# Optimization experiments

Measured on AMD Instinct MI355X. Metric: run time of the kernel, lower is better.

The kernel has to match this reference:

```python
import jax, jax.numpy as jnp
import numpy as np
from jax import lax

B, C, H, W = 4, 256, 64, 64
C8 = C // 8  # 32


def setup_inputs() -> dict:
    key = jax.random.key(0)
    ks = jax.random.split(key, 8)
    x = jax.random.normal(ks[0], (B, C, H, W), jnp.float32)
    # 1x1 conv weights stored as [out_ch, in_ch]
    wb = jax.random.normal(ks[1], (C8, 2 * C), jnp.float32) * 0.02
    bb = jax.random.normal(ks[2], (C8,), jnp.float32) * 0.02
    wc = jax.random.normal(ks[3], (C8, 2 * C), jnp.float32) * 0.02
    bc = jax.random.normal(ks[4], (C8,), jnp.float32) * 0.02
    wd = jax.random.normal(ks[5], (C, 2 * C), jnp.float32) * 0.02
    bd = jax.random.normal(ks[6], (C,), jnp.float32) * 0.02
    alpha = jnp.float32(0.5)  # nn.Parameter(zeros(1)) at init; nonzero for a meaningful test
    return {"x": x, "wb": wb, "bb": bb, "wc": wc, "bc": bc, "wd": wd, "bd": bd, "alpha": alpha}


def reference(x, wb, bb, wc, bc, wd, bd, alpha):
    b, c, h, w = x.shape
    n = h * w
    pad = [(0, 0), (0, 0), (1, 1), (1, 1)]
    # F.avg_pool2d(k=3, s=1, p=1) with count_include_pad=True -> window-sum / 9
    x_avg = lax.reduce_window(x, 0.0, lax.add, (1, 1, 3, 3), (1, 1, 1, 1), pad) / 9.0
    x_max = lax.reduce_window(x, -jnp.inf, lax.max, (1, 1, 3, 3), (1, 1, 1, 1), pad)
    cat = jnp.concatenate([x_avg, x_max], axis=1)  # [B, 2C, H, W]
    catf = cat.reshape(b, 2 * c, n)                # [B, 2C, N]
    # 1x1 convs == per-pixel linear projections
    feat_b = jnp.einsum('oc,bcn->bon', wb, catf) + bb[None, :, None]  # [B, C8, N]
    feat_c = jnp.einsum('oc,bcn->bon', wc, catf) + bc[None, :, None]  # [B, C8, N]
    feat_d = jnp.einsum('oc,bcn->bon', wd, catf) + bd[None, :, None]  # [B, C,  N]
    # attention_s = softmax(feat_b^T @ feat_c) over last dim -> [B, N, N]
    attn = jax.nn.softmax(jnp.einsum('bon,bom->bnm', feat_b, feat_c), axis=-1)
    # feat_e = feat_d @ attn^T -> [B, C, N]
    feat_e = jnp.einsum('bcn,bmn->bcm', feat_d, attn).reshape(b, c, h, w)
    return alpha * feat_e + (1.0 - alpha) * x
```

## Files before the change

### kernel.cpp

```cpp
#include <hip/hip_runtime.h>
#include <hip/hip_bf16.h>

typedef __hip_bfloat16 bf16;
typedef __attribute__((ext_vector_type(8))) short s8v;
typedef __attribute__((ext_vector_type(4))) float f4v;

__device__ __forceinline__ ushort f2u(float f) {
    bf16 h = __float2bfloat16(f);
    return *(ushort*)&h;
}


__global__ __launch_bounds__(256) void wcvt_kernel(
    const float* __restrict__ wb, const float* __restrict__ wc,
    const float* __restrict__ wd, ushort* __restrict__ Wf) {
    int f = blockIdx.x * 4 + (threadIdx.x >> 6);
    int l = threadIdx.x & 63;
    int ot = f % 20, kc = f / 20;
    int o = ot * 16 + (l & 15);
    int k0 = kc * 32 + (l >> 4) * 8;
    const float* wr = (o < 32) ? wb + (size_t)o * 512
                    : (o < 64) ? wc + (size_t)(o - 32) * 512
                               : wd + (size_t)(o - 64) * 512;
    float4 f0 = *(const float4*)(wr + k0);
    float4 f1 = *(const float4*)(wr + k0 + 4);
    ushort tmp[8] = {f2u(f0.x), f2u(f0.y), f2u(f0.z), f2u(f0.w),
                     f2u(f1.x), f2u(f1.y), f2u(f1.z), f2u(f1.w)};
    *(uint4*)(Wf + kc * 10240 + ot * 512 + l * 8) = *(uint4*)tmp;
}

__global__ __launch_bounds__(512, 2) void fused_kernel(
    const float* __restrict__ x, const ushort* __restrict__ Wf,
    const float* __restrict__ bb, const float* __restrict__ bc,
    const float* __restrict__ bd,
    ushort* __restrict__ Qb, ushort* __restrict__ Kb, ushort* __restrict__ Vf) {
    __shared__ __align__(16) char smem[117248];
    float*  Xs   = (float*)smem;
    ushort* Vls  = (ushort*)smem;
    ushort* catS = (ushort*)(smem + 50688);

    int tid = threadIdx.x;
    int bid = blockIdx.x;
    int lb = (bid & 7) * 32 + (bid >> 3);
    int b = lb >> 6, h = lb & 63;
    bool hasU = (h > 0), hasD = (h < 63);

    float4 xr[6];
#define LOADCG(CG)                                                              \
    {                                                                           \
        _Pragma("unroll")                                                       \
        for (int pp = 0; pp < 6; ++pp) {                                        \
            int linear = pp * 512 + tid;                                        \
            int w4 = linear & 15, cs_s = (linear >> 4) & 63, dh = linear >> 10; \
            int hh = h + dh - 1;                                                \
            float4 fv = {0.f, 0.f, 0.f, 0.f};                                   \
            if ((unsigned)hh < 64u)                                             \
                fv = *(const float4*)(x + ((size_t)(b * 256 + (CG) * 64 + cs_s)) * 4096 \
                                      + hh * 64 + w4 * 4);                      \
            xr[pp] = fv;                                                        \
        }                                                                       \
    }
    LOADCG(0)
    #pragma unroll
    for (int cg = 0; cg < 4; ++cg) {
        #pragma unroll
        for (int pp = 0; pp < 6; ++pp) {
            int linear = pp * 512 + tid;
            int w4 = linear & 15, cs_s = (linear >> 4) & 63, dh = linear >> 10;
            float* xp = Xs + (dh * 64 + w4 * 4) * 66 + cs_s;
            xp[0]   = xr[pp].x;
            xp[66]  = xr[pp].y;
            xp[132] = xr[pp].z;
            xp[198] = xr[pp].w;
        }
        __syncthreads();
        if (cg == 0) LOADCG(1)
        else if (cg == 1) LOADCG(2)
        else if (cg == 2) LOADCG(3)
        {
            int cs = tid & 63, wsw = tid >> 6;
            float vs[10], vm[10];
            #pragma unroll
            for (int j = 0; j < 10; ++j) {
                int w = wsw * 8 - 1 + j;
                if ((unsigned)w < 64u) {
                    float u = Xs[w * 66 + cs];
                    float m = Xs[(64 + w) * 66 + cs];
                    float d = Xs[(128 + w) * 66 + cs];
                    vs[j] = u + m + d;
                    float mx = m;
                    if (hasU) mx = fmaxf(mx, u);
                    if (hasD) mx = fmaxf(mx, d);
                    vm[j] = mx;
                } else { vs[j] = 0.f; vm[j] = -3.4e38f; }
            }
            int chb = cg * 64 + cs;
            #pragma unroll
            for (int i = 0; i < 8; ++i) {
                float sum = vs[i] + vs[i + 1] + vs[i + 2];
                float mx  = fmaxf(fmaxf(vm[i], vm[i + 1]), vm[i + 2]);
                catS[(wsw * 8 + i) * 520 + chb]       = f2u(sum * (1.f / 9.f));
                catS[(wsw * 8 + i) * 520 + 256 + chb] = f2u(mx);
            }
        }
        __syncthreads();
    }
#undef LOADCG

    int l = tid & 63, w = tid >> 6;
    int lm = l & 15, q = l >> 4;
    int nc = w & 3, oh = w >> 2;
    f4v pacc[10];
    #pragma unroll
    for (int ot = 0; ot < 10; ++ot)
        #pragma unroll
        for (int i = 0; i < 4; ++i) pacc[ot][i] = 0.f;

    const ushort* wfp = Wf + (oh * 10) * 512 + l * 8;
    const ushort* ap  = catS + (nc * 16 + lm) * 520 + q * 8;
    #pragma unroll 2
    for (int kci = 0; kci < 16; ++kci) {
        s8v Af = *(const s8v*)(ap + kci * 32);
        s8v Bf[10];
        #pragma unroll
        for (int ot = 0; ot < 10; ++ot)
            Bf[ot] = *(const s8v*)(wfp + kci * 10240 + ot * 512);
        #pragma unroll
        for (int ot = 0; ot < 10; ++ot)
            pacc[ot] = __builtin_amdgcn_mfma_f32_16x16x32_bf16(Af, Bf[ot], pacc[ot], 0, 0, 0);
    }

    size_t nrow = (size_t)((b << 12) + h * 64 + nc * 16 + q * 4);
    if (oh == 0) {
        #pragma unroll
        for (int ot = 0; ot < 2; ++ot) {
            int o = ot * 16 + lm;
            float bias = bb[o];
            #pragma unroll
            for (int r = 0; r < 4; ++r)
                Qb[(nrow + r) * 32 + o] = f2u(pacc[ot][r] + bias);
        }
        #pragma unroll
        for (int ot = 2; ot < 4; ++ot) {
            int o = ot * 16 + lm - 32;
            float bias = bc[o];
            #pragma unroll
            for (int r = 0; r < 4; ++r)
                Kb[(nrow + r) * 32 + o] = f2u(pacc[ot][r] + bias);
        }
        #pragma unroll
        for (int ot = 4; ot < 10; ++ot) {
            int c = ot * 16 + lm - 64;
            float bias = bd[c];
            ushort tmp[4];
            #pragma unroll
            for (int r = 0; r < 4; ++r) tmp[r] = f2u(pacc[ot][r] + bias);
            *(uint2*)&Vls[c * 72 + nc * 16 + q * 4] = *(uint2*)tmp;
        }
    } else {
        #pragma unroll
        for (int ot = 0; ot < 10; ++ot) {
            int c = 96 + ot * 16 + lm;
            float bias = bd[c];
            ushort tmp[4];
            #pragma unroll
            for (int r = 0; r < 4; ++r) tmp[r] = f2u(pacc[ot][r] + bias);
            *(uint2*)&Vls[c * 72 + nc * 16 + q * 4] = *(uint2*)tmp;
        }
    }
    __syncthreads();
    {
        size_t vb = ((size_t)b << 20) + (size_t)(h * 2) * 8192 + l * 8;
        #pragma unroll
        for (int i = 0; i < 2; ++i) {
            int cb = w * 2 + i;
            #pragma unroll
            for (int nh = 0; nh < 2; ++nh)
                *(uint4*)(Vf + vb + nh * 8192 + cb * 512)
                    = *(const uint4*)&Vls[(cb * 16 + lm) * 72 + nh * 32 + q * 8];
        }
    }
}

__global__ __launch_bounds__(512, 2) void attn_kernel(
    const ushort* __restrict__ Qb, const ushort* __restrict__ Kb,
    const ushort* __restrict__ Vf, const float* __restrict__ x,
    const float* __restrict__ alphap, float* __restrict__ out) {
    __shared__ __align__(16) ushort Ps[2][64][72];
    __shared__ float Obuf[4][64][17];
    __shared__ float Lpart[4][64];
    __shared__ float Lrow[64];
    int tid = threadIdx.x;
    int l = tid & 63, w = tid >> 6;
    int lm = l & 15, q = l >> 4;
    int nsw = w & 3, kh = w >> 2;
    int bid = blockIdx.x;
    int xcd = bid & 7;
    int b = xcd & 3;
    int midx = (bid >> 3) + ((xcd >> 2) << 5);
    int m0 = midx << 6;
    size_t bN = (size_t)b << 12;

    s8v Qf[2];
    {
        const ushort* qb = Qb + (bN + m0 + kh * 32) * 32;
        Qf[0] = *(const s8v*)(qb + (size_t)(lm) * 32 + q * 8);
        Qf[1] = *(const s8v*)(qb + (size_t)(16 + lm) * 32 + q * 8);
    }
    const ushort* kbp = Kb + (bN + nsw * 16 + lm) * 32 + q * 8;
    const ushort* vfp = Vf + ((size_t)b << 20) + kh * 8192 + (nsw * 4) * 512 + l * 8;

    f4v acc[4][4];
    #pragma unroll
    for (int mt = 0; mt < 4; ++mt)
        #pragma unroll
        for (int ct = 0; ct < 4; ++ct)
            #pragma unroll
            for (int i = 0; i < 4; ++i) acc[mt][ct][i] = 0.f;
    float La0 = 0.f, La1 = 0.f;

    s8v kf0 = *(const s8v*)kbp;
    s8v kf1 = *(const s8v*)(kbp + 2048);
    s8v vfA[4], vfB[4];
    #pragma unroll
    for (int ct = 0; ct < 4; ++ct) vfA[ct] = *(const s8v*)(vfp + ct * 512);
    {
        f4v S0 = {0.f, 0.f, 0.f, 0.f}, S1 = {0.f, 0.f, 0.f, 0.f};
        S0 = __builtin_amdgcn_mfma_f32_16x16x32_bf16(kf0, Qf[0], S0, 0, 0, 0);
        S1 = __builtin_amdgcn_mfma_f32_16x16x32_bf16(kf0, Qf[1], S1, 0, 0, 0);
        ushort e0[4], e1[4];
        #pragma unroll
        for (int r = 0; r < 4; ++r) {
            float f0 = __expf(fminf(S0[r], 60.f));
            float f1 = __expf(fminf(S1[r], 60.f));
            La0 += f0; La1 += f1;
            e0[r] = f2u(f0); e1[r] = f2u(f1);
        }
        *(uint2*)&Ps[0][kh * 32 + lm][nsw * 16 + q * 4]      = *(uint2*)e0;
        *(uint2*)&Ps[0][kh * 32 + 16 + lm][nsw * 16 + q * 4] = *(uint2*)e1;
    }
    __syncthreads();

#define TILE_BODY(TT, KFS, KFP, VCUR, VNXT)                                       \
    {                                                                             \
        int p = (TT) & 1;                                                         \
        if ((TT) < 62) KFP = *(const s8v*)(kbp + (size_t)((TT) + 2) * 2048);      \
        if ((TT) < 63) {                                                          \
            const ushort* vn = vfp + (size_t)((TT) + 1) * 16384;                  \
            _Pragma("unroll")                                                     \
            for (int ct = 0; ct < 4; ++ct)                                        \
                VNXT[ct] = *(const s8v*)(vn + ct * 512);                          \
        }                                                                         \
        f4v S0 = {0.f, 0.f, 0.f, 0.f}, S1 = {0.f, 0.f, 0.f, 0.f};                 \
        if ((TT) < 63) {                                                          \
            S0 = __builtin_amdgcn_mfma_f32_16x16x32_bf16(KFS, Qf[0], S0, 0, 0, 0);\
            S1 = __builtin_amdgcn_mfma_f32_16x16x32_bf16(KFS, Qf[1], S1, 0, 0, 0);\
        }                                                                         \
        s8v Af0 = *(const s8v*)&Ps[p][lm][kh * 32 + q * 8];                       \
        s8v Af1 = *(const s8v*)&Ps[p][16 + lm][kh * 32 + q * 8];                  \
        s8v Af2 = *(const s8v*)&Ps[p][32 + lm][kh * 32 + q * 8];                  \
        s8v Af3 = *(const s8v*)&Ps[p][48 + lm][kh * 32 + q * 8];                  \
        if ((TT) < 63) {                                                          \
            ushort e0[4], e1[4];                                                  \
            _Pragma("unroll")                                                     \
            for (int r = 0; r < 4; ++r) {                                         \
                float f0 = __expf(fminf(S0[r], 60.f));                            \
                float f1 = __expf(fminf(S1[r], 60.f));                            \
                La0 += f0; La1 += f1;                                             \
                e0[r] = f2u(f0); e1[r] = f2u(f1);                                 \
            }                                                                     \
            *(uint2*)&Ps[1 - p][kh * 32 + lm][nsw * 16 + q * 4]      = *(uint2*)e0;\
            *(uint2*)&Ps[1 - p][kh * 32 + 16 + lm][nsw * 16 + q * 4] = *(uint2*)e1;\
        }                                                                         \
        _Pragma("unroll")                                                         \
        for (int ct = 0; ct < 4; ++ct) {                                          \
            acc[0][ct] = __builtin_amdgcn_mfma_f32_16x16x32_bf16(Af0, VCUR[ct], acc[0][ct], 0, 0, 0); \
            acc[1][ct] = __builtin_amdgcn_mfma_f32_16x16x32_bf16(Af1, VCUR[ct], acc[1][ct], 0, 0, 0); \
            acc[2][ct] = __builtin_amdgcn_mfma_f32_16x16x32_bf16(Af2, VCUR[ct], acc[2][ct], 0, 0, 0); \
            acc[3][ct] = __builtin_amdgcn_mfma_f32_16x16x32_bf16(Af3, VCUR[ct], acc[3][ct], 0, 0, 0); \
        }                                                                         \
        asm volatile("s_waitcnt lgkmcnt(0)\n\ts_barrier" ::: "memory");           \
    }

    for (int t = 0; t < 64; t += 2) {
        TILE_BODY(t,     kf1, kf0, vfA, vfB);
        TILE_BODY(t + 1, kf0, kf1, vfB, vfA);
    }
#undef TILE_BODY

    La0 += __shfl_xor(La0, 16, 64); La0 += __shfl_xor(La0, 32, 64);
    La1 += __shfl_xor(La1, 16, 64); La1 += __shfl_xor(La1, 32, 64);
    if (q == 0) {
        Lpart[nsw][kh * 32 + lm]      = La0;
        Lpart[nsw][kh * 32 + 16 + lm] = La1;
    }
    __syncthreads();
    if (tid < 64)
        Lrow[tid] = Lpart[0][tid] + Lpart[1][tid] + Lpart[2][tid] + Lpart[3][tid];
    __syncthreads();
    #pragma unroll
    for (int ct = 0; ct < 4; ++ct) {
        if (kh == 1) {
            #pragma unroll
            for (int mt = 0; mt < 4; ++mt)
                #pragma unroll
                for (int r = 0; r < 4; ++r)
                    Obuf[nsw][mt * 16 + q * 4 + r][lm] = acc[mt][ct][r];
        }
        __syncthreads();
        if (kh == 0) {
            #pragma unroll
            for (int mt = 0; mt < 4; ++mt)
                #pragma unroll
                for (int r = 0; r < 4; ++r)
                    acc[mt][ct][r] += Obuf[nsw][mt * 16 + q * 4 + r][lm];
        }
        __syncthreads();
    }
    if (kh == 0) {
        float alpha = alphap[0];
        float ra = 1.f - alpha;
        #pragma unroll
        for (int mt = 0; mt < 4; ++mt) {
            float L0 = Lrow[mt * 16 + q * 4 + 0];
            float L1 = Lrow[mt * 16 + q * 4 + 1];
            float L2 = Lrow[mt * 16 + q * 4 + 2];
            float L3 = Lrow[mt * 16 + q * 4 + 3];
            #pragma unroll
            for (int ct = 0; ct < 4; ++ct) {
                int cc = nsw * 64 + ct * 16 + lm;
                size_t base = ((size_t)(b * 256 + cc)) * 4096 + m0 + mt * 16 + q * 4;
                float4 xv = *(const float4*)(x + base);
                float4 ov;
                ov.x = alpha * (acc[mt][ct][0] / L0) + ra * xv.x;
                ov.y = alpha * (acc[mt][ct][1] / L1) + ra * xv.y;
                ov.z = alpha * (acc[mt][ct][2] / L2) + ra * xv.z;
                ov.w = alpha * (acc[mt][ct][3] / L3) + ra * xv.w;
                *(float4*)(out + base) = ov;
            }
        }
    }
}

extern "C" void kernel_launch(void* const* d_in, const int* in_sizes, int n_in,
                              void* d_out, int out_size, void* d_ws, size_t ws_size,
                              hipStream_t stream) {
    const float* x  = (const float*)d_in[0];
    const float* wb = (const float*)d_in[1];
    const float* bb = (const float*)d_in[2];
    const float* wc = (const float*)d_in[3];
    const float* bc = (const float*)d_in[4];
    const float* wd = (const float*)d_in[5];
    const float* bd = (const float*)d_in[6];
    const float* al = (const float*)d_in[7];
    float* out = (float*)d_out;

    char* ws = (char*)d_ws;
    ushort* Qb = (ushort*)ws;
    ushort* Kb = (ushort*)(ws + 1048576);
    ushort* Vf = (ushort*)(ws + 2097152);
    ushort* Wf = (ushort*)(ws + 10485760);

    wcvt_kernel<<<dim3(80), dim3(256), 0, stream>>>(wb, wc, wd, Wf);
    fused_kernel<<<dim3(256), dim3(512), 0, stream>>>(x, Wf, bb, bc, bd,
                                                      Qb, Kb, Vf);
    attn_kernel<<<dim3(256), dim3(512), 0, stream>>>(Qb, Kb, Vf, x, al, out);
}
```

Before: 164.2 us.

## Merge three kernels into one cooperative kernel with grid-wide syncs

```diff
diff --git a/kernel.cpp b/kernel.cpp
--- a/kernel.cpp
+++ b/kernel.cpp
@@ -1,5 +1,8 @@
 #include <hip/hip_runtime.h>
 #include <hip/hip_bf16.h>
+#include <hip/hip_cooperative_groups.h>
+
+namespace cg = cooperative_groups;
 
 typedef __hip_bfloat16 bf16;
 typedef __attribute__((ext_vector_type(8))) short s8v;
@@ -10,6 +13,345 @@
     return *(ushort*)&h;
 }
 
+
+__global__ __launch_bounds__(512, 2) void mega_kernel(
+    const float* __restrict__ x,
+    const float* __restrict__ wb, const float* __restrict__ bb,
+    const float* __restrict__ wc, const float* __restrict__ bc,
+    const float* __restrict__ wd, const float* __restrict__ bd,
+    const float* __restrict__ alphap,
+    ushort* __restrict__ Qb, ushort* __restrict__ Kb,
+    ushort* __restrict__ Vf, ushort* __restrict__ Wf,
+    float* __restrict__ out) {
+    cg::grid_group grid = cg::this_grid();
+    __shared__ __align__(16) char smem[117248];
+    int tid = threadIdx.x;
+    int bid = blockIdx.x;
+
+    if (bid < 40) {
+        int f = bid * 8 + (tid >> 6);
+        int l = tid & 63;
+        int ot = f % 20, kc = f / 20;
+        int o = ot * 16 + (l & 15);
+        int k0 = kc * 32 + (l >> 4) * 8;
+        const float* wr = (o < 32) ? wb + (size_t)o * 512
+                        : (o < 64) ? wc + (size_t)(o - 32) * 512
+                                   : wd + (size_t)(o - 64) * 512;
+        float4 f0 = *(const float4*)(wr + k0);
+        float4 f1 = *(const float4*)(wr + k0 + 4);
+        ushort tmp[8] = {f2u(f0.x), f2u(f0.y), f2u(f0.z), f2u(f0.w),
+                         f2u(f1.x), f2u(f1.y), f2u(f1.z), f2u(f1.w)};
+        *(uint4*)(Wf + kc * 10240 + ot * 512 + l * 8) = *(uint4*)tmp;
+    }
+    __threadfence();
+    grid.sync();
+    __threadfence();
+
+    {
+        float*  Xs   = (float*)smem;
+        ushort* Vls  = (ushort*)smem;
+        ushort* catS = (ushort*)(smem + 50688);
+
+        int lb = (bid & 7) * 32 + (bid >> 3);
+        int b = lb >> 6, h = lb & 63;
+        bool hasU = (h > 0), hasD = (h < 63);
+
+        float4 xr[6];
+#define LOADCG(CG)                                                              \
+        {                                                                       \
+            _Pragma("unroll")                                                   \
+            for (int pp = 0; pp < 6; ++pp) {                                    \
+                int linear = pp * 512 + tid;                                    \
+                int w4 = linear & 15, cs_s = (linear >> 4) & 63, dh = linear >> 10; \
+                int hh = h + dh - 1;                                            \
+                float4 fv = {0.f, 0.f, 0.f, 0.f};                               \
+                if ((unsigned)hh < 64u)                                         \
+                    fv = *(const float4*)(x + ((size_t)(b * 256 + (CG) * 64 + cs_s)) * 4096 \
+                                          + hh * 64 + w4 * 4);                  \
+                xr[pp] = fv;                                                    \
+            }                                                                   \
+        }
+        LOADCG(0)
+        #pragma unroll
+        for (int cg_i = 0; cg_i < 4; ++cg_i) {
+            #pragma unroll
+            for (int pp = 0; pp < 6; ++pp) {
+                int linear = pp * 512 + tid;
+                int w4 = linear & 15, cs_s = (linear >> 4) & 63, dh = linear >> 10;
+                float* xp = Xs + (dh * 64 + w4 * 4) * 66 + cs_s;
+                xp[0]   = xr[pp].x;
+                xp[66]  = xr[pp].y;
+                xp[132] = xr[pp].z;
+                xp[198] = xr[pp].w;
+            }
+            __syncthreads();
+            if (cg_i == 0) LOADCG(1)
+            else if (cg_i == 1) LOADCG(2)
+            else if (cg_i == 2) LOADCG(3)
+            {
+                int cs = tid & 63, wsw = tid >> 6;
+                float vs[10], vm[10];
+                #pragma unroll
+                for (int j = 0; j < 10; ++j) {
+                    int w = wsw * 8 - 1 + j;
+                    if ((unsigned)w < 64u) {
+                        float u = Xs[w * 66 + cs];
+                        float m = Xs[(64 + w) * 66 + cs];
+                        float d = Xs[(128 + w) * 66 + cs];
+                        vs[j] = u + m + d;
+                        float mx = m;
+                        if (hasU) mx = fmaxf(mx, u);
+                        if (hasD) mx = fmaxf(mx, d);
+                        vm[j] = mx;
+                    } else { vs[j] = 0.f; vm[j] = -3.4e38f; }
+                }
+                int chb = cg_i * 64 + cs;
+                #pragma unroll
+                for (int i = 0; i < 8; ++i) {
+                    float sum = vs[i] + vs[i + 1] + vs[i + 2];
+                    float mx  = fmaxf(fmaxf(vm[i], vm[i + 1]), vm[i + 2]);
+                    catS[(wsw * 8 + i) * 520 + chb]       = f2u(sum * (1.f / 9.f));
+                    catS[(wsw * 8 + i) * 520 + 256 + chb] = f2u(mx);
+                }
+            }
+            __syncthreads();
+        }
+#undef LOADCG
+
+        int l = tid & 63, w = tid >> 6;
+        int lm = l & 15, q = l >> 4;
+        int nc = w & 3, oh = w >> 2;
+        f4v pacc[10];
+        #pragma unroll
+        for (int ot = 0; ot < 10; ++ot)
+            #pragma unroll
+            for (int i = 0; i < 4; ++i) pacc[ot][i] = 0.f;
+
+        const ushort* wfp = Wf + (oh * 10) * 512 + l * 8;
+        const ushort* ap  = catS + (nc * 16 + lm) * 520 + q * 8;
+        #pragma unroll 2
+        for (int kci = 0; kci < 16; ++kci) {
+            s8v Af = *(const s8v*)(ap + kci * 32);
+            s8v Bf[10];
+            #pragma unroll
+            for (int ot = 0; ot < 10; ++ot)
+                Bf[ot] = *(const s8v*)(wfp + kci * 10240 + ot * 512);
+            #pragma unroll
+            for (int ot = 0; ot < 10; ++ot)
+                pacc[ot] = __builtin_amdgcn_mfma_f32_16x16x32_bf16(Af, Bf[ot], pacc[ot], 0, 0, 0);
+        }
+
+        size_t nrow = (size_t)((b << 12) + h * 64 + nc * 16 + q * 4);
+        if (oh == 0) {
+            #pragma unroll
+            for (int ot = 0; ot < 2; ++ot) {
+                int o = ot * 16 + lm;
+                float bias = bb[o];
+                #pragma unroll
+                for (int r = 0; r < 4; ++r)
+                    Qb[(nrow + r) * 32 + o] = f2u(pacc[ot][r] + bias);
+            }
+            #pragma unroll
+            for (int ot = 2; ot < 4; ++ot) {
+                int o = ot * 16 + lm - 32;
+                float bias = bc[o];
+                #pragma unroll
+                for (int r = 0; r < 4; ++r)
+                    Kb[(nrow + r) * 32 + o] = f2u(pacc[ot][r] + bias);
+            }
+            #pragma unroll
+            for (int ot = 4; ot < 10; ++ot) {
+                int c = ot * 16 + lm - 64;
+                float bias = bd[c];
+                ushort tmp[4];
+                #pragma unroll
+                for (int r = 0; r < 4; ++r) tmp[r] = f2u(pacc[ot][r] + bias);
+                *(uint2*)&Vls[c * 72 + nc * 16 + q * 4] = *(uint2*)tmp;
+            }
+        } else {
+            #pragma unroll
+            for (int ot = 0; ot < 10; ++ot) {
+                int c = 96 + ot * 16 + lm;
+                float bias = bd[c];
+                ushort tmp[4];
+                #pragma unroll
+                for (int r = 0; r < 4; ++r) tmp[r] = f2u(pacc[ot][r] + bias);
+                *(uint2*)&Vls[c * 72 + nc * 16 + q * 4] = *(uint2*)tmp;
+            }
+        }
+        __syncthreads();
+        {
+            size_t vb = ((size_t)b << 20) + (size_t)(h * 2) * 8192 + l * 8;
+            #pragma unroll
+            for (int i = 0; i < 2; ++i) {
+                int cb = w * 2 + i;
+                #pragma unroll
+                for (int nh = 0; nh < 2; ++nh)
+                    *(uint4*)(Vf + vb + nh * 8192 + cb * 512)
+                        = *(const uint4*)&Vls[(cb * 16 + lm) * 72 + nh * 32 + q * 8];
+            }
+        }
+    }
+    __threadfence();
+    grid.sync();
+    __threadfence();
+
+    {
+        ushort* Ps   = (ushort*)smem;
+        float*  Obuf = (float*)(smem + 18432);
+        float*  Lpart= (float*)(smem + 35840);
+        float*  Lrow = (float*)(smem + 36864);
+
+        int l = tid & 63, w = tid >> 6;
+        int lm = l & 15, q = l >> 4;
+        int nsw = w & 3, kh = w >> 2;
+        int xcd = bid & 7;
+        int b = xcd & 3;
+        int midx = (bid >> 3) + ((xcd >> 2) << 5);
+        int m0 = midx << 6;
+        size_t bN = (size_t)b << 12;
+
+        s8v Qf[2];
+        {
+            const ushort* qb = Qb + (bN + m0 + kh * 32) * 32;
+            Qf[0] = *(const s8v*)(qb + (size_t)(lm) * 32 + q * 8);
+            Qf[1] = *(const s8v*)(qb + (size_t)(16 + lm) * 32 + q * 8);
+        }
+        const ushort* kbp = Kb + (bN + nsw * 16 + lm) * 32 + q * 8;
+        const ushort* vfp = Vf + ((size_t)b << 20) + kh * 8192 + (nsw * 4) * 512 + l * 8;
+
+        f4v acc[4][4];
+        #pragma unroll
+        for (int mt = 0; mt < 4; ++mt)
+            #pragma unroll
+            for (int ct = 0; ct < 4; ++ct)
+                #pragma unroll
+                for (int i = 0; i < 4; ++i) acc[mt][ct][i] = 0.f;
+        float La0 = 0.f, La1 = 0.f;
+
+        s8v kf0 = *(const s8v*)kbp;
+        s8v kf1 = *(const s8v*)(kbp + 2048);
+        s8v vfA[4], vfB[4];
+        #pragma unroll
+        for (int ct = 0; ct < 4; ++ct) vfA[ct] = *(const s8v*)(vfp + ct * 512);
+        {
+            f4v S0 = {0.f, 0.f, 0.f, 0.f}, S1 = {0.f, 0.f, 0.f, 0.f};
+            S0 = __builtin_amdgcn_mfma_f32_16x16x32_bf16(kf0, Qf[0], S0, 0, 0, 0);
+            S1 = __builtin_amdgcn_mfma_f32_16x16x32_bf16(kf0, Qf[1], S1, 0, 0, 0);
+            ushort e0[4], e1[4];
+            #pragma unroll
+            for (int r = 0; r < 4; ++r) {
+                float f0 = __expf(fminf(S0[r], 60.f));
+                float f1 = __expf(fminf(S1[r], 60.f));
+                La0 += f0; La1 += f1;
+                e0[r] = f2u(f0); e1[r] = f2u(f1);
+            }
+            *(uint2*)(Ps + (kh * 32 + lm) * 72 + nsw * 16 + q * 4)      = *(uint2*)e0;
+            *(uint2*)(Ps + (kh * 32 + 16 + lm) * 72 + nsw * 16 + q * 4) = *(uint2*)e1;
+        }
+        __syncthreads();
+
+#define TILE_BODY(TT, KFS, KFP, VCUR, VNXT)                                       \
+    {                                                                             \
+        int p = (TT) & 1;                                                         \
+        if ((TT) < 62) KFP = *(const s8v*)(kbp + (size_t)((TT) + 2) * 2048);      \
+        if ((TT) < 63) {                                                          \
+            const ushort* vn = vfp + (size_t)((TT) + 1) * 16384;                  \
+            _Pragma("unroll")                                                     \
+            for (int ct = 0; ct < 4; ++ct)                                        \
+                VNXT[ct] = *(const s8v*)(vn + ct * 512);                          \
+        }                                                                         \
+        f4v S0 = {0.f, 0.f, 0.f, 0.f}, S1 = {0.f, 0.f, 0.f, 0.f};                 \
+        if ((TT) < 63) {                                                          \
+            S0 = __builtin_amdgcn_mfma_f32_16x16x32_bf16(KFS, Qf[0], S0, 0, 0, 0);\
+            S1 = __builtin_amdgcn_mfma_f32_16x16x32_bf16(KFS, Qf[1], S1, 0, 0, 0);\
+        }                                                                         \
+        s8v Af0 = *(const s8v*)(Ps + p * 4608 + (lm) * 72 + kh * 32 + q * 8);     \
+        s8v Af1 = *(const s8v*)(Ps + p * 4608 + (16 + lm) * 72 + kh * 32 + q * 8);\
+        s8v Af2 = *(const s8v*)(Ps + p * 4608 + (32 + lm) * 72 + kh * 32 + q * 8);\
+        s8v Af3 = *(const s8v*)(Ps + p * 4608 + (48 + lm) * 72 + kh * 32 + q * 8);\
+        if ((TT) < 63) {                                                          \
+            ushort e0[4], e1[4];                                                  \
+            _Pragma("unroll")                                                     \
+            for (int r = 0; r < 4; ++r) {                                         \
+                float f0 = __expf(fminf(S0[r], 60.f));                            \
+                float f1 = __expf(fminf(S1[r], 60.f));                            \
+                La0 += f0; La1 += f1;                                             \
+                e0[r] = f2u(f0); e1[r] = f2u(f1);                                 \
+            }                                                                     \
+            *(uint2*)(Ps + (1 - p) * 4608 + (kh * 32 + lm) * 72 + nsw * 16 + q * 4)      = *(uint2*)e0; \
+            *(uint2*)(Ps + (1 - p) * 4608 + (kh * 32 + 16 + lm) * 72 + nsw * 16 + q * 4) = *(uint2*)e1; \
+        }                                                                         \
+        _Pragma("unroll")                                                         \
+        for (int ct = 0; ct < 4; ++ct) {                                          \
+            acc[0][ct] = __builtin_amdgcn_mfma_f32_16x16x32_bf16(Af0, VCUR[ct], acc[0][ct], 0, 0, 0); \
+            acc[1][ct] = __builtin_amdgcn_mfma_f32_16x16x32_bf16(Af1, VCUR[ct], acc[1][ct], 0, 0, 0); \
+            acc[2][ct] = __builtin_amdgcn_mfma_f32_16x16x32_bf16(Af2, VCUR[ct], acc[2][ct], 0, 0, 0); \
+            acc[3][ct] = __builtin_amdgcn_mfma_f32_16x16x32_bf16(Af3, VCUR[ct], acc[3][ct], 0, 0, 0); \
+        }                                                                         \
+        asm volatile("s_waitcnt lgkmcnt(0)\n\ts_barrier" ::: "memory");           \
+    }
+
+        for (int t = 0; t < 64; t += 2) {
+            TILE_BODY(t,     kf1, kf0, vfA, vfB);
+            TILE_BODY(t + 1, kf0, kf1, vfB, vfA);
+        }
+#undef TILE_BODY
+
+        La0 += __shfl_xor(La0, 16, 64); La0 += __shfl_xor(La0, 32, 64);
+        La1 += __shfl_xor(La1, 16, 64); La1 += __shfl_xor(La1, 32, 64);
+        if (q == 0) {
+            Lpart[nsw * 64 + kh * 32 + lm]      = La0;
+            Lpart[nsw * 64 + kh * 32 + 16 + lm] = La1;
+        }
+        __syncthreads();
+        if (tid < 64)
+            Lrow[tid] = Lpart[tid] + Lpart[64 + tid] + Lpart[128 + tid] + Lpart[192 + tid];
+        __syncthreads();
+        #pragma unroll
+        for (int ct = 0; ct < 4; ++ct) {
+            if (kh == 1) {
+                #pragma unroll
+                for (int mt = 0; mt < 4; ++mt)
+                    #pragma unroll
+                    for (int r = 0; r < 4; ++r)
+                        Obuf[nsw * 1088 + (mt * 16 + q * 4 + r) * 17 + lm] = acc[mt][ct][r];
+            }
+            __syncthreads();
+            if (kh == 0) {
+                #pragma unroll
+                for (int mt = 0; mt < 4; ++mt)
+                    #pragma unroll
+                    for (int r = 0; r < 4; ++r)
+                        acc[mt][ct][r] += Obuf[nsw * 1088 + (mt * 16 + q * 4 + r) * 17 + lm];
+            }
+            __syncthreads();
+        }
+        if (kh == 0) {
+            float alpha = alphap[0];
+            float ra = 1.f - alpha;
+            #pragma unroll
+            for (int mt = 0; mt < 4; ++mt) {
+                float L0 = Lrow[mt * 16 + q * 4 + 0];
+                float L1 = Lrow[mt * 16 + q * 4 + 1];
+                float L2 = Lrow[mt * 16 + q * 4 + 2];
+                float L3 = Lrow[mt * 16 + q * 4 + 3];
+                #pragma unroll
+                for (int ct = 0; ct < 4; ++ct) {
+                    int cc = nsw * 64 + ct * 16 + lm;
+                    size_t base = ((size_t)(b * 256 + cc)) * 4096 + m0 + mt * 16 + q * 4;
+                    float4 xv = *(const float4*)(x + base);
+                    float4 ov;
+                    ov.x = alpha * (acc[mt][ct][0] / L0) + ra * xv.x;
+                    ov.y = alpha * (acc[mt][ct][1] / L1) + ra * xv.y;
+                    ov.z = alpha * (acc[mt][ct][2] / L2) + ra * xv.z;
+                    ov.w = alpha * (acc[mt][ct][3] / L3) + ra * xv.w;
+                    *(float4*)(out + base) = ov;
+                }
+            }
+        }
+    }
+}
 
 __global__ __launch_bounds__(256) void wcvt_kernel(
     const float* __restrict__ wb, const float* __restrict__ wc,
@@ -361,8 +703,15 @@
     ushort* Vf = (ushort*)(ws + 2097152);
     ushort* Wf = (ushort*)(ws + 10485760);
 
-    wcvt_kernel<<<dim3(80), dim3(256), 0, stream>>>(wb, wc, wd, Wf);
-    fused_kernel<<<dim3(256), dim3(512), 0, stream>>>(x, Wf, bb, bc, bd,
-                                                      Qb, Kb, Vf);
-    attn_kernel<<<dim3(256), dim3(512), 0, stream>>>(Qb, Kb, Vf, x, al, out);
+    void* kargs[] = {(void*)&x, (void*)&wb, (void*)&bb, (void*)&wc, (void*)&bc,
+                     (void*)&wd, (void*)&bd, (void*)&al, (void*)&Qb, (void*)&Kb,
+                     (void*)&Vf, (void*)&Wf, (void*)&out};
+    hipError_t err = hipLaunchCooperativeKernel((void*)mega_kernel, dim3(256),
+                                                dim3(512), kargs, 0, stream);
+    if (err != hipSuccess) {
+        wcvt_kernel<<<dim3(80), dim3(256), 0, stream>>>(wb, wc, wd, Wf);
+        fused_kernel<<<dim3(256), dim3(512), 0, stream>>>(x, Wf, bb, bc, bd,
+                                                          Qb, Kb, Vf);
+        attn_kernel<<<dim3(256), dim3(512), 0, stream>>>(Qb, Kb, Vf, x, al, out);
+    }
 }
```

Result: slower. 363.2 us (+121.1%).

## Double key tile width per iteration in attention loop to halve barriers

Applied to the files above, without the earlier changes.

```diff
diff --git a/kernel.cpp b/kernel.cpp
--- a/kernel.cpp
+++ b/kernel.cpp
@@ -186,7 +186,7 @@
     const ushort* __restrict__ Qb, const ushort* __restrict__ Kb,
     const ushort* __restrict__ Vf, const float* __restrict__ x,
     const float* __restrict__ alphap, float* __restrict__ out) {
-    __shared__ __align__(16) ushort Ps[2][64][72];
+    __shared__ __align__(16) ushort Ps[2][64][136];
     __shared__ float Obuf[4][64][17];
     __shared__ float Lpart[4][64];
     __shared__ float Lrow[64];
@@ -207,8 +207,9 @@
         Qf[0] = *(const s8v*)(qb + (size_t)(lm) * 32 + q * 8);
         Qf[1] = *(const s8v*)(qb + (size_t)(16 + lm) * 32 + q * 8);
     }
-    const ushort* kbp = Kb + (bN + nsw * 16 + lm) * 32 + q * 8;
-    const ushort* vfp = Vf + ((size_t)b << 20) + kh * 8192 + (nsw * 4) * 512 + l * 8;
+    const ushort* kbp = Kb + (bN + nsw * 32 + lm) * 32 + q * 8;
+    const ushort* vfp = Vf + ((size_t)b << 20) + (size_t)(2 * kh) * 8192
+                        + (nsw * 4) * 512 + l * 8;
 
     f4v acc[4][4];
     #pragma unroll
@@ -219,74 +220,90 @@
             for (int i = 0; i < 4; ++i) acc[mt][ct][i] = 0.f;
     float La0 = 0.f, La1 = 0.f;
 
-    s8v kf0 = *(const s8v*)kbp;
-    s8v kf1 = *(const s8v*)(kbp + 2048);
-    s8v vfA[4], vfB[4];
-    #pragma unroll
-    for (int ct = 0; ct < 4; ++ct) vfA[ct] = *(const s8v*)(vfp + ct * 512);
+#define SCORE_TAIL(S00, S01, S10, S11, PDST)                                      \
+    {                                                                             \
+        ushort e00[4], e01[4], e10[4], e11[4];                                    \
+        _Pragma("unroll")                                                         \
+        for (int r = 0; r < 4; ++r) {                                             \
+            float f00 = __expf(fminf(S00[r], 60.f));                              \
+            float f01 = __expf(fminf(S01[r], 60.f));                              \
+            float f10 = __expf(fminf(S10[r], 60.f));                              \
+            float f11 = __expf(fminf(S11[r], 60.f));                              \
+            La0 += f00 + f10; La1 += f01 + f11;                                   \
+            e00[r] = f2u(f00); e01[r] = f2u(f01);                                 \
+            e10[r] = f2u(f10); e11[r] = f2u(f11);                                 \
+        }                                                                         \
+        *(uint2*)&PDST[kh * 32 + lm][nsw * 32 + q * 4]           = *(uint2*)e00;  \
+        *(uint2*)&PDST[kh * 32 + 16 + lm][nsw * 32 + q * 4]      = *(uint2*)e01;  \
+        *(uint2*)&PDST[kh * 32 + lm][nsw * 32 + 16 + q * 4]      = *(uint2*)e10;  \
+        *(uint2*)&PDST[kh * 32 + 16 + lm][nsw * 32 + 16 + q * 4] = *(uint2*)e11;  \
+    }
+
+    s8v kfA[2], kfB[2], vfA[8], vfB[8];
+    kfA[0] = *(const s8v*)(kbp);
+    kfA[1] = *(const s8v*)(kbp + 512);
+    kfB[0] = *(const s8v*)(kbp + 4096);
+    kfB[1] = *(const s8v*)(kbp + 4096 + 512);
+    #pragma unroll
+    for (int i = 0; i < 8; ++i)
+        vfA[i] = *(const s8v*)(vfp + (i >> 1) * 512 + (i & 1) * 8192);
     {
-        f4v S0 = {0.f, 0.f, 0.f, 0.f}, S1 = {0.f, 0.f, 0.f, 0.f};
-        S0 = __builtin_amdgcn_mfma_f32_16x16x32_bf16(kf0, Qf[0], S0, 0, 0, 0);
-        S1 = __builtin_amdgcn_mfma_f32_16x16x32_bf16(kf0, Qf[1], S1, 0, 0, 0);
-        ushort e0[4], e1[4];
-        #pragma unroll
-        for (int r = 0; r < 4; ++r) {
-            float f0 = __expf(fminf(S0[r], 60.f));
-            float f1 = __expf(fminf(S1[r], 60.f));
-            La0 += f0; La1 += f1;
-            e0[r] = f2u(f0); e1[r] = f2u(f1);
-        }
-        *(uint2*)&Ps[0][kh * 32 + lm][nsw * 16 + q * 4]      = *(uint2*)e0;
-        *(uint2*)&Ps[0][kh * 32 + 16 + lm][nsw * 16 + q * 4] = *(uint2*)e1;
+        f4v S00 = {0.f, 0.f, 0.f, 0.f}, S01 = {0.f, 0.f, 0.f, 0.f};
+        f4v S10 = {0.f, 0.f, 0.f, 0.f}, S11 = {0.f, 0.f, 0.f, 0.f};
+        S00 = __builtin_amdgcn_mfma_f32_16x16x32_bf16(kfA[0], Qf[0], S00, 0, 0, 0);
+        S01 = __builtin_amdgcn_mfma_f32_16x16x32_bf16(kfA[0], Qf[1], S01, 0, 0, 0);
+        S10 = __builtin_amdgcn_mfma_f32_16x16x32_bf16(kfA[1], Qf[0], S10, 0, 0, 0);
+        S11 = __builtin_amdgcn_mfma_f32_16x16x32_bf16(kfA[1], Qf[1], S11, 0, 0, 0);
+        SCORE_TAIL(S00, S01, S10, S11, Ps[0])
     }
     __syncthreads();
 
 #define TILE_BODY(TT, KFS, KFP, VCUR, VNXT)                                       \
     {                                                                             \
         int p = (TT) & 1;                                                         \
-        if ((TT) < 62) KFP = *(const s8v*)(kbp + (size_t)((TT) + 2) * 2048);      \
-        if ((TT) < 63) {                                                          \
-            const ushort* vn = vfp + (size_t)((TT) + 1) * 16384;                  \
+        if ((TT) < 30) {                                                          \
+            const ushort* kn = kbp + (size_t)((TT) + 2) * 4096;                   \
+            KFP[0] = *(const s8v*)kn;                                             \
+            KFP[1] = *(const s8v*)(kn + 512);                                     \
+        }                                                                         \
+        if ((TT) < 31) {                                                          \
+            const ushort* vn = vfp + (size_t)((TT) + 1) * 32768;                  \
             _Pragma("unroll")                                                     \
-            for (int ct = 0; ct < 4; ++ct)                                        \
-                VNXT[ct] = *(const s8v*)(vn + ct * 512);                          \
-        }                                                                         \
-        f4v S0 = {0.f, 0.f, 0.f, 0.f}, S1 = {0.f, 0.f, 0.f, 0.f};                 \
-        if ((TT) < 63) {                                                          \
-            S0 = __builtin_amdgcn_mfma_f32_16x16x32_bf16(KFS, Qf[0], S0, 0, 0, 0);\
-            S1 = __builtin_amdgcn_mfma_f32_16x16x32_bf16(KFS, Qf[1], S1, 0, 0, 0);\
-        }                                                                         \
-        s8v Af0 = *(const s8v*)&Ps[p][lm][kh * 32 + q * 8];                       \
-        s8v Af1 = *(const s8v*)&Ps[p][16 + lm][kh * 32 + q * 8];                  \
-        s8v Af2 = *(const s8v*)&Ps[p][32 + lm][kh * 32 + q * 8];                  \
-        s8v Af3 = *(const s8v*)&Ps[p][48 + lm][kh * 32 + q * 8];                  \
-        if ((TT) < 63) {                                                          \
-            ushort e0[4], e1[4];                                                  \
-            _Pragma("unroll")                                                     \
-            for (int r = 0; r < 4; ++r) {                                         \
-                float f0 = __expf(fminf(S0[r], 60.f));                            \
-                float f1 = __expf(fminf(S1[r], 60.f));                            \
-                La0 += f0; La1 += f1;                                             \
-                e0[r] = f2u(f0); e1[r] = f2u(f1);                                 \
-            }                                                                     \
-            *(uint2*)&Ps[1 - p][kh * 32 + lm][nsw * 16 + q * 4]      = *(uint2*)e0;\
-            *(uint2*)&Ps[1 - p][kh * 32 + 16 + lm][nsw * 16 + q * 4] = *(uint2*)e1;\
-        }                                                                         \
+            for (int i = 0; i < 8; ++i)                                           \
+                VNXT[i] = *(const s8v*)(vn + (i >> 1) * 512 + (i & 1) * 8192);    \
+        }                                                                         \
+        f4v S00 = {0.f, 0.f, 0.f, 0.f}, S01 = {0.f, 0.f, 0.f, 0.f};               \
+        f4v S10 = {0.f, 0.f, 0.f, 0.f}, S11 = {0.f, 0.f, 0.f, 0.f};               \
+        if ((TT) < 31) {                                                          \
+            S00 = __builtin_amdgcn_mfma_f32_16x16x32_bf16(KFS[0], Qf[0], S00, 0, 0, 0); \
+            S01 = __builtin_amdgcn_mfma_f32_16x16x32_bf16(KFS[0], Qf[1], S01, 0, 0, 0); \
+            S10 = __builtin_amdgcn_mfma_f32_16x16x32_bf16(KFS[1], Qf[0], S10, 0, 0, 0); \
+            S11 = __builtin_amdgcn_mfma_f32_16x16x32_bf16(KFS[1], Qf[1], S11, 0, 0, 0); \
+        }                                                                         \
+        s8v Af[4][2];                                                             \
+        _Pragma("unroll")                                                         \
+        for (int mt = 0; mt < 4; ++mt) {                                          \
+            Af[mt][0] = *(const s8v*)&Ps[p][mt * 16 + lm][kh * 64 + q * 8];       \
+            Af[mt][1] = *(const s8v*)&Ps[p][mt * 16 + lm][kh * 64 + 32 + q * 8];  \
+        }                                                                         \
+        if ((TT) < 31) SCORE_TAIL(S00, S01, S10, S11, Ps[1 - p])                  \
         _Pragma("unroll")                                                         \
         for (int ct = 0; ct < 4; ++ct) {                                          \
-            acc[0][ct] = __builtin_amdgcn_mfma_f32_16x16x32_bf16(Af0, VCUR[ct], acc[0][ct], 0, 0, 0); \
-            acc[1][ct] = __builtin_amdgcn_mfma_f32_16x16x32_bf16(Af1, VCUR[ct], acc[1][ct], 0, 0, 0); \
-            acc[2][ct] = __builtin_amdgcn_mfma_f32_16x16x32_bf16(Af2, VCUR[ct], acc[2][ct], 0, 0, 0); \
-            acc[3][ct] = __builtin_amdgcn_mfma_f32_16x16x32_bf16(Af3, VCUR[ct], acc[3][ct], 0, 0, 0); \
+            _Pragma("unroll")                                                     \
+            for (int mt = 0; mt < 4; ++mt) {                                      \
+                acc[mt][ct] = __builtin_amdgcn_mfma_f32_16x16x32_bf16(Af[mt][0], VCUR[ct * 2],     acc[mt][ct], 0, 0, 0); \
+                acc[mt][ct] = __builtin_amdgcn_mfma_f32_16x16x32_bf16(Af[mt][1], VCUR[ct * 2 + 1], acc[mt][ct], 0, 0, 0); \
+            }                                                                     \
         }                                                                         \
         asm volatile("s_waitcnt lgkmcnt(0)\n\ts_barrier" ::: "memory");           \
     }
 
-    for (int t = 0; t < 64; t += 2) {
-        TILE_BODY(t,     kf1, kf0, vfA, vfB);
-        TILE_BODY(t + 1, kf0, kf1, vfB, vfA);
+    for (int t = 0; t < 32; t += 2) {
+        TILE_BODY(t,     kfB, kfA, vfA, vfB);
+        TILE_BODY(t + 1, kfA, kfB, vfB, vfA);
     }
 #undef TILE_BODY
+#undef SCORE_TAIL
 
     La0 += __shfl_xor(La0, 16, 64); La0 += __shfl_xor(La0, 32, 64);
     La1 += __shfl_xor(La1, 16, 64); La1 += __shfl_xor(La1, 32, 64);
```

After: 158.3 us. 1.04x faster.

## Enlarge attention key tile to 256 to cut barrier and loop overhead

Applied to the files above, without the earlier changes.

```diff
diff --git a/kernel.cpp b/kernel.cpp
--- a/kernel.cpp
+++ b/kernel.cpp
@@ -186,7 +186,7 @@
     const ushort* __restrict__ Qb, const ushort* __restrict__ Kb,
     const ushort* __restrict__ Vf, const float* __restrict__ x,
     const float* __restrict__ alphap, float* __restrict__ out) {
-    __shared__ __align__(16) ushort Ps[2][64][72];
+    __shared__ __align__(16) ushort Ps[2][64][260];
     __shared__ float Obuf[4][64][17];
     __shared__ float Lpart[4][64];
     __shared__ float Lrow[64];
@@ -207,8 +207,9 @@
         Qf[0] = *(const s8v*)(qb + (size_t)(lm) * 32 + q * 8);
         Qf[1] = *(const s8v*)(qb + (size_t)(16 + lm) * 32 + q * 8);
     }
-    const ushort* kbp = Kb + (bN + nsw * 16 + lm) * 32 + q * 8;
-    const ushort* vfp = Vf + ((size_t)b << 20) + kh * 8192 + (nsw * 4) * 512 + l * 8;
+    const ushort* kbp = Kb + (bN + nsw * 64 + lm) * 32 + q * 8;
+    const ushort* vfp = Vf + ((size_t)b << 20) + (size_t)(4 * kh) * 8192
+                        + (nsw * 4) * 512 + l * 8;
 
     f4v acc[4][4];
     #pragma unroll
@@ -219,74 +220,89 @@
             for (int i = 0; i < 4; ++i) acc[mt][ct][i] = 0.f;
     float La0 = 0.f, La1 = 0.f;
 
-    s8v kf0 = *(const s8v*)kbp;
-    s8v kf1 = *(const s8v*)(kbp + 2048);
-    s8v vfA[4], vfB[4];
-    #pragma unroll
-    for (int ct = 0; ct < 4; ++ct) vfA[ct] = *(const s8v*)(vfp + ct * 512);
+#define SCORE_ONE(SC0, SC1, CC, PDST)                                             \
+    {                                                                             \
+        ushort e0[4], e1[4];                                                      \
+        _Pragma("unroll")                                                         \
+        for (int r = 0; r < 4; ++r) {                                             \
+            float f0 = __expf(fminf(SC0[r], 60.f));                               \
+            float f1 = __expf(fminf(SC1[r], 60.f));                               \
+            La0 += f0; La1 += f1;                                                 \
+            e0[r] = f2u(f0); e1[r] = f2u(f1);                                     \
+        }                                                                         \
+        *(uint2*)&PDST[kh * 32 + lm][nsw * 64 + (CC) * 16 + q * 4]      = *(uint2*)e0; \
+        *(uint2*)&PDST[kh * 32 + 16 + lm][nsw * 64 + (CC) * 16 + q * 4] = *(uint2*)e1; \
+    }
+
+    s8v kfA[4], kfB[4];
+    #pragma unroll
+    for (int c = 0; c < 4; ++c) kfA[c] = *(const s8v*)(kbp + c * 512);
+    #pragma unroll
+    for (int c = 0; c < 4; ++c) kfB[c] = *(const s8v*)(kbp + 8192 + c * 512);
     {
-        f4v S0 = {0.f, 0.f, 0.f, 0.f}, S1 = {0.f, 0.f, 0.f, 0.f};
-        S0 = __builtin_amdgcn_mfma_f32_16x16x32_bf16(kf0, Qf[0], S0, 0, 0, 0);
-        S1 = __builtin_amdgcn_mfma_f32_16x16x32_bf16(kf0, Qf[1], S1, 0, 0, 0);
-        ushort e0[4], e1[4];
-        #pragma unroll
-        for (int r = 0; r < 4; ++r) {
-            float f0 = __expf(fminf(S0[r], 60.f));
-            float f1 = __expf(fminf(S1[r], 60.f));
-            La0 += f0; La1 += f1;
-            e0[r] = f2u(f0); e1[r] = f2u(f1);
-        }
-        *(uint2*)&Ps[0][kh * 32 + lm][nsw * 16 + q * 4]      = *(uint2*)e0;
-        *(uint2*)&Ps[0][kh * 32 + 16 + lm][nsw * 16 + q * 4] = *(uint2*)e1;
+        #pragma unroll
+        for (int c = 0; c < 4; ++c) {
+            f4v S0 = {0.f, 0.f, 0.f, 0.f}, S1 = {0.f, 0.f, 0.f, 0.f};
+            S0 = __builtin_amdgcn_mfma_f32_16x16x32_bf16(kfA[c], Qf[0], S0, 0, 0, 0);
+            S1 = __builtin_amdgcn_mfma_f32_16x16x32_bf16(kfA[c], Qf[1], S1, 0, 0, 0);
+            SCORE_ONE(S0, S1, c, Ps[0])
+        }
     }
     __syncthreads();
 
-#define TILE_BODY(TT, KFS, KFP, VCUR, VNXT)                                       \
+#define TILE_BODY(TT, KFS, KFP)                                                   \
     {                                                                             \
         int p = (TT) & 1;                                                         \
-        if ((TT) < 62) KFP = *(const s8v*)(kbp + (size_t)((TT) + 2) * 2048);      \
-        if ((TT) < 63) {                                                          \
-            const ushort* vn = vfp + (size_t)((TT) + 1) * 16384;                  \
-            _Pragma("unroll")                                                     \
-            for (int ct = 0; ct < 4; ++ct)                                        \
-                VNXT[ct] = *(const s8v*)(vn + ct * 512);                          \
-        }                                                                         \
-        f4v S0 = {0.f, 0.f, 0.f, 0.f}, S1 = {0.f, 0.f, 0.f, 0.f};                 \
-        if ((TT) < 63) {                                                          \
-            S0 = __builtin_amdgcn_mfma_f32_16x16x32_bf16(KFS, Qf[0], S0, 0, 0, 0);\
-            S1 = __builtin_amdgcn_mfma_f32_16x16x32_bf16(KFS, Qf[1], S1, 0, 0, 0);\
-        }                                                                         \
-        s8v Af0 = *(const s8v*)&Ps[p][lm][kh * 32 + q * 8];                       \
-        s8v Af1 = *(const s8v*)&Ps[p][16 + lm][kh * 32 + q * 8];                  \
-        s8v Af2 = *(const s8v*)&Ps[p][32 + lm][kh * 32 + q * 8];                  \
-        s8v Af3 = *(const s8v*)&Ps[p][48 + lm][kh * 32 + q * 8];                  \
-        if ((TT) < 63) {                                                          \
-            ushort e0[4], e1[4];                                                  \
-            _Pragma("unroll")                                                     \
-            for (int r = 0; r < 4; ++r) {                                         \
-                float f0 = __expf(fminf(S0[r], 60.f));                            \
-                float f1 = __expf(fminf(S1[r], 60.f));                            \
-                La0 += f0; La1 += f1;                                             \
-                e0[r] = f2u(f0); e1[r] = f2u(f1);                                 \
+        s8v vf[16];                                                               \
+        {                                                                         \
+            const ushort* vt = vfp + (size_t)(TT) * 65536;                        \
+            _Pragma("unroll")                                                     \
+            for (int i = 0; i < 16; ++i)                                          \
+                vf[i] = *(const s8v*)(vt + (i >> 2) * 8192 + (i & 3) * 512);      \
+        }                                                                         \
+        if ((TT) < 14) {                                                          \
+            const ushort* kn = kbp + (size_t)((TT) + 2) * 8192;                   \
+            _Pragma("unroll")                                                     \
+            for (int c = 0; c < 4; ++c) KFP[c] = *(const s8v*)(kn + c * 512);     \
+        }                                                                         \
+        f4v S[4][2];                                                              \
+        if ((TT) < 15) {                                                          \
+            _Pragma("unroll")                                                     \
+            for (int c = 0; c < 4; ++c) {                                         \
+                _Pragma("unroll")                                                 \
+                for (int h = 0; h < 2; ++h) {                                     \
+                    S[c][h][0] = 0.f; S[c][h][1] = 0.f;                           \
+                    S[c][h][2] = 0.f; S[c][h][3] = 0.f;                           \
+                    S[c][h] = __builtin_amdgcn_mfma_f32_16x16x32_bf16(            \
+                        KFS[c], Qf[h], S[c][h], 0, 0, 0);                         \
+                }                                                                 \
             }                                                                     \
-            *(uint2*)&Ps[1 - p][kh * 32 + lm][nsw * 16 + q * 4]      = *(uint2*)e0;\
-            *(uint2*)&Ps[1 - p][kh * 32 + 16 + lm][nsw * 16 + q * 4] = *(uint2*)e1;\
+            _Pragma("unroll")                                                     \
+            for (int c = 0; c < 4; ++c) SCORE_ONE(S[c][0], S[c][1], c, Ps[1 - p]) \
         }                                                                         \
         _Pragma("unroll")                                                         \
-        for (int ct = 0; ct < 4; ++ct) {                                          \
-            acc[0][ct] = __builtin_amdgcn_mfma_f32_16x16x32_bf16(Af0, VCUR[ct], acc[0][ct], 0, 0, 0); \
-            acc[1][ct] = __builtin_amdgcn_mfma_f32_16x16x32_bf16(Af1, VCUR[ct], acc[1][ct], 0, 0, 0); \
-            acc[2][ct] = __builtin_amdgcn_mfma_f32_16x16x32_bf16(Af2, VCUR[ct], acc[2][ct], 0, 0, 0); \
-            acc[3][ct] = __builtin_amdgcn_mfma_f32_16x16x32_bf16(Af3, VCUR[ct], acc[3][ct], 0, 0, 0); \
+        for (int ks = 0; ks < 4; ++ks) {                                          \
+            s8v Af[4];                                                            \
+            _Pragma("unroll")                                                     \
+            for (int mt = 0; mt < 4; ++mt)                                        \
+                Af[mt] = *(const s8v*)&Ps[p][mt * 16 + lm][kh * 128 + ks * 32 + q * 8]; \
+            _Pragma("unroll")                                                     \
+            for (int ct = 0; ct < 4; ++ct) {                                      \
+                _Pragma("unroll")                                                 \
+                for (int mt = 0; mt < 4; ++mt)                                    \
+                    acc[mt][ct] = __builtin_amdgcn_mfma_f32_16x16x32_bf16(        \
+                        Af[mt], vf[ks * 4 + ct], acc[mt][ct], 0, 0, 0);           \
+            }                                                                     \
         }                                                                         \
         asm volatile("s_waitcnt lgkmcnt(0)\n\ts_barrier" ::: "memory");           \
     }
 
-    for (int t = 0; t < 64; t += 2) {
-        TILE_BODY(t,     kf1, kf0, vfA, vfB);
-        TILE_BODY(t + 1, kf0, kf1, vfB, vfA);
+    for (int t = 0; t < 16; t += 2) {
+        TILE_BODY(t,     kfB, kfA);
+        TILE_BODY(t + 1, kfA, kfB);
     }
 #undef TILE_BODY
+#undef SCORE_ONE
 
     La0 += __shfl_xor(La0, 16, 64); La0 += __shfl_xor(La0, 32, 64);
     La1 += __shfl_xor(La1, 16, 64); La1 += __shfl_xor(La1, 32, 64);
```

Measured after the change: 158.8 us. -3.3%, faster.
